# Performance work log

Hardware: AMD Instinct MI355X
Metric: run time of the kernel (lower is better)

## Reference

```python
import jax, jax.numpy as jnp
import numpy as np

B = 4096      # number of queries
N = 65536     # number of reference points

def setup_inputs() -> dict:
    key = jax.random.key(0)
    k1, k2, k3 = jax.random.split(key, 3)
    x = jax.random.normal(k1, (B,), dtype=jnp.float32)
    input_tensor = jax.random.normal(k2, (N,), dtype=jnp.float32)
    accuracy_tensor = jax.random.uniform(k3, (N,), dtype=jnp.float32)
    return {"x": x, "input_tensor": input_tensor, "accuracy_tensor": accuracy_tensor}

def reference(x, input_tensor, accuracy_tensor):
    # (B, N) broadcast abs-difference distance matrix
    distances = jnp.abs(input_tensor[None, :] - x[:, None])
    # nearest reference point per query
    min_idx = jnp.argmin(distances, axis=1)          # (B,)
    return accuracy_tensor[min_idx]                  # (B,)
```

## Files before the change

### kernel.cpp

```cpp
#include <hip/hip_runtime.h>

#define CHUNK 512
#define GRP   32
#define Q     2
#define QB    4

__global__ __launch_bounds__(256, 8)
void nn_init_kernel(unsigned long long* __restrict__ best, int B) {
    int i = blockIdx.x * 256 + threadIdx.x;
    if (i < B) best[i] = ~0ULL;
}

__global__ __launch_bounds__(256, 8)
void nn_main_kernel(const float* __restrict__ x,
                    const float* __restrict__ pts,
                    unsigned long long* __restrict__ best,
                    int qg_shift)
{
    __shared__ float lds[CHUNK];
    const int tid = threadIdx.x;
    const int qg = blockIdx.x & ((1 << qg_shift) - 1);
    const int ck = blockIdx.x >> qg_shift;

    reinterpret_cast<float2*>(lds)[tid] =
        reinterpret_cast<const float2*>(pts)[ck * (CHUNK / 2) + tid];

    const int q0 = (qg << 9) + tid;
    const float xq0 = x[q0];
    const float xq1 = x[q0 + 256];

    __syncthreads();

    const float inf = __builtin_inff();
    float bdA0 = inf, bdB0 = inf, prev0 = inf;
    float bdA1 = inf, bdB1 = inf, prev1 = inf;
    int grp0 = 0, grp1 = 0;

    const float4* __restrict__ l4 = reinterpret_cast<const float4*>(lds);

    #pragma unroll 2
    for (int g = 0; g < CHUNK / GRP; ++g) {
        #pragma unroll
        for (int t = 0; t < GRP / 4; ++t) {
            float4 v = l4[g * (GRP / 4) + t];
            bdA0 = fminf(fminf(fabsf(v.x - xq0), fabsf(v.y - xq0)), bdA0);
            bdB0 = fminf(fminf(fabsf(v.z - xq0), fabsf(v.w - xq0)), bdB0);
            bdA1 = fminf(fminf(fabsf(v.x - xq1), fabsf(v.y - xq1)), bdA1);
            bdB1 = fminf(fminf(fabsf(v.z - xq1), fabsf(v.w - xq1)), bdB1);
        }
        float cur0 = fminf(bdA0, bdB0);
        float cur1 = fminf(bdA1, bdB1);
        grp0 = (cur0 < prev0) ? g : grp0;  prev0 = cur0;
        grp1 = (cur1 < prev1) ? g : grp1;  prev1 = cur1;
    }

    int bi0 = 0, bi1 = 0;
    const float4* __restrict__ pg0 = l4 + grp0 * (GRP / 4);
    const float4* __restrict__ pg1 = l4 + grp1 * (GRP / 4);
    #pragma unroll
    for (int t = GRP / 4 - 1; t >= 0; --t) {
        float4 v = pg0[t];
        bi0 = (fabsf(v.w - xq0) == prev0) ? 4 * t + 3 : bi0;
        bi0 = (fabsf(v.z - xq0) == prev0) ? 4 * t + 2 : bi0;
        bi0 = (fabsf(v.y - xq0) == prev0) ? 4 * t + 1 : bi0;
        bi0 = (fabsf(v.x - xq0) == prev0) ? 4 * t + 0 : bi0;
    }
    #pragma unroll
    for (int t = GRP / 4 - 1; t >= 0; --t) {
        float4 v = pg1[t];
        bi1 = (fabsf(v.w - xq1) == prev1) ? 4 * t + 3 : bi1;
        bi1 = (fabsf(v.z - xq1) == prev1) ? 4 * t + 2 : bi1;
        bi1 = (fabsf(v.y - xq1) == prev1) ? 4 * t + 1 : bi1;
        bi1 = (fabsf(v.x - xq1) == prev1) ? 4 * t + 0 : bi1;
    }

    const unsigned base = (unsigned)(ck * CHUNK);
    const unsigned long long key0 =
        ((unsigned long long)__float_as_uint(prev0) << 32) |
        (base + (unsigned)(grp0 * GRP + bi0));
    const unsigned long long key1 =
        ((unsigned long long)__float_as_uint(prev1) << 32) |
        (base + (unsigned)(grp1 * GRP + bi1));
    atomicMin(&best[q0], key0);
    atomicMin(&best[q0 + 256], key1);
}

__global__ __launch_bounds__(256, 8)
void nn_gather_kernel(const unsigned long long* __restrict__ best,
                      const float* __restrict__ acc,
                      float* __restrict__ out, int B) {
    int i = blockIdx.x * 256 + threadIdx.x;
    if (i < B) out[i] = acc[(unsigned)(best[i] & 0xffffffffULL)];
}

__global__ __launch_bounds__(256, 4)
void nn_kernel(const float* __restrict__ x,
               const float* __restrict__ pts,
               const float* __restrict__ acc,
               float* __restrict__ out,
               int B, int N) {
    const int lane = threadIdx.x & 63;
    const int wave = threadIdx.x >> 6;
    const int q    = blockIdx.x * QB + wave;
    if (q >= B) return;

    const float xq = x[q];
    const int G = N >> 2;
    const int J = G >> 6;

    float bd0 = __builtin_inff(), bd1 = __builtin_inff(),
          bd2 = __builtin_inff(), bd3 = __builtin_inff();
    int   bj0 = 0, bj1 = 0, bj2 = 0, bj3 = 0;

    const float4* __restrict__ p4 = reinterpret_cast<const float4*>(pts);

    #pragma unroll 4
    for (int j = 0; j < J; ++j) {
        float4 v = p4[lane + 64 * j];
        float d0 = fabsf(v.x - xq);
        float d1 = fabsf(v.y - xq);
        float d2 = fabsf(v.z - xq);
        float d3 = fabsf(v.w - xq);
        if (d0 < bd0) { bd0 = d0; bj0 = j; }
        if (d1 < bd1) { bd1 = d1; bj1 = j; }
        if (d2 < bd2) { bd2 = d2; bj2 = j; }
        if (d3 < bd3) { bd3 = d3; bj3 = j; }
    }

    unsigned long long key;
    {
        unsigned i0 = (unsigned)(4 * (lane + 64 * bj0) + 0);
        unsigned i1 = (unsigned)(4 * (lane + 64 * bj1) + 1);
        unsigned i2 = (unsigned)(4 * (lane + 64 * bj2) + 2);
        unsigned i3 = (unsigned)(4 * (lane + 64 * bj3) + 3);
        unsigned long long k0 = ((unsigned long long)__float_as_uint(bd0) << 32) | i0;
        unsigned long long k1 = ((unsigned long long)__float_as_uint(bd1) << 32) | i1;
        unsigned long long k2 = ((unsigned long long)__float_as_uint(bd2) << 32) | i2;
        unsigned long long k3 = ((unsigned long long)__float_as_uint(bd3) << 32) | i3;
        key = k0 < k1 ? k0 : k1;
        unsigned long long k23 = k2 < k3 ? k2 : k3;
        key = key < k23 ? key : k23;
    }

    for (int i = J * 256 + lane; i < N; i += 64) {
        float d = fabsf(pts[i] - xq);
        unsigned long long k = ((unsigned long long)__float_as_uint(d) << 32) | (unsigned)i;
        key = key < k ? key : k;
    }

    #pragma unroll
    for (int off = 1; off < 64; off <<= 1) {
        unsigned long long o = __shfl_xor(key, off, 64);
        key = key < o ? key : o;
    }

    if (lane == 0) {
        out[q] = acc[(unsigned)(key & 0xffffffffULL)];
    }
}

extern "C" void kernel_launch(void* const* d_in, const int* in_sizes, int n_in,
                              void* d_out, int out_size, void* d_ws, size_t ws_size,
                              hipStream_t stream) {
    const float* x   = (const float*)d_in[0];
    const float* pts = (const float*)d_in[1];
    const float* acc = (const float*)d_in[2];
    float* out = (float*)d_out;
    const int B = in_sizes[0];
    const int N = in_sizes[1];

    const int nqg = B >> 9;
    const bool pow2 = (nqg > 0) && ((nqg & (nqg - 1)) == 0);
    const bool fast = pow2 && (B % 512 == 0) && (N % CHUNK == 0) &&
                      d_ws != nullptr && ws_size >= (size_t)B * 8;

    if (fast) {
        int qg_shift = 0;
        while ((1 << qg_shift) < nqg) ++qg_shift;
        const int nchunk = N / CHUNK;
        unsigned long long* best = (unsigned long long*)d_ws;

        hipLaunchKernelGGL(nn_init_kernel, dim3((B + 255) / 256), dim3(256), 0,
                           stream, best, B);
        hipLaunchKernelGGL(nn_main_kernel, dim3(nchunk * nqg), dim3(256), 0,
                           stream, x, pts, best, qg_shift);
        hipLaunchKernelGGL(nn_gather_kernel, dim3((B + 255) / 256), dim3(256),
                           0, stream, best, acc, out, B);
    } else {
        const int blocks = (B + QB - 1) / QB;
        hipLaunchKernelGGL(nn_kernel, dim3(blocks), dim3(256), 0, stream,
                           x, pts, acc, out, B, N);
    }
}
```

Before: 71.88 us.

## Replace global atomicMin with per-chunk partial buffer and separate reduction kernel

The main kernel now writes each chunk's best key into a per-chunk partial array instead of doing 64-bit atomicMin on a shared best array, and a new reduce kernel scans all chunks per query and gathers the accuracy value. This drops the init kernel and the atomic contention but requires nchunk*B*8 bytes of workspace, 128 chunks times 4096 queries, about 4 MB. The reduce kernel launches only 64 blocks of 64 threads, each thread doing 128 serial loads, so it may be latency bound. If the workspace is too small the fast path is not taken and the slow fallback kernel runs.

```diff
diff --git a/kernel.cpp b/kernel.cpp
--- a/kernel.cpp
+++ b/kernel.cpp
@@ -2,20 +2,13 @@
 
 #define CHUNK 512
 #define GRP   32
-#define Q     2
 #define QB    4
 
-__global__ __launch_bounds__(256, 8)
-void nn_init_kernel(unsigned long long* __restrict__ best, int B) {
-    int i = blockIdx.x * 256 + threadIdx.x;
-    if (i < B) best[i] = ~0ULL;
-}
-
-__global__ __launch_bounds__(256, 8)
+__global__ __launch_bounds__(256, 4)
 void nn_main_kernel(const float* __restrict__ x,
                     const float* __restrict__ pts,
-                    unsigned long long* __restrict__ best,
-                    int qg_shift)
+                    unsigned long long* __restrict__ part,
+                    int B, int qg_shift)
 {
     __shared__ float lds[CHUNK];
     const int tid = threadIdx.x;
@@ -81,16 +74,27 @@
     const unsigned long long key1 =
         ((unsigned long long)__float_as_uint(prev1) << 32) |
         (base + (unsigned)(grp1 * GRP + bi1));
-    atomicMin(&best[q0], key0);
-    atomicMin(&best[q0 + 256], key1);
+
+    part[(size_t)ck * B + q0]       = key0;
+    part[(size_t)ck * B + q0 + 256] = key1;
 }
 
-__global__ __launch_bounds__(256, 8)
-void nn_gather_kernel(const unsigned long long* __restrict__ best,
+__global__ __launch_bounds__(64, 8)
+void nn_reduce_kernel(const unsigned long long* __restrict__ part,
                       const float* __restrict__ acc,
-                      float* __restrict__ out, int B) {
-    int i = blockIdx.x * 256 + threadIdx.x;
-    if (i < B) out[i] = acc[(unsigned)(best[i] & 0xffffffffULL)];
+                      float* __restrict__ out,
+                      int B, int nchunk)
+{
+    const int q = blockIdx.x * 64 + threadIdx.x;
+    if (q >= B) return;
+
+    unsigned long long key = ~0ULL;
+    #pragma unroll 8
+    for (int c = 0; c < nchunk; ++c) {
+        unsigned long long k = part[(size_t)c * B + q];
+        key = k < key ? k : key;
+    }
+    out[q] = acc[(unsigned)(key & 0xffffffffULL)];
 }
 
 __global__ __launch_bounds__(256, 4)
@@ -170,22 +174,21 @@
     const int N = in_sizes[1];
 
     const int nqg = B >> 9;
+    const int nchunk = N / CHUNK;
     const bool pow2 = (nqg > 0) && ((nqg & (nqg - 1)) == 0);
     const bool fast = pow2 && (B % 512 == 0) && (N % CHUNK == 0) &&
-                      d_ws != nullptr && ws_size >= (size_t)B * 8;
+                      d_ws != nullptr &&
+                      ws_size >= (size_t)nchunk * (size_t)B * 8;
 
     if (fast) {
         int qg_shift = 0;
         while ((1 << qg_shift) < nqg) ++qg_shift;
-        const int nchunk = N / CHUNK;
-        unsigned long long* best = (unsigned long long*)d_ws;
+        unsigned long long* part = (unsigned long long*)d_ws;
 
-        hipLaunchKernelGGL(nn_init_kernel, dim3((B + 255) / 256), dim3(256), 0,
-                           stream, best, B);
         hipLaunchKernelGGL(nn_main_kernel, dim3(nchunk * nqg), dim3(256), 0,
-                           stream, x, pts, best, qg_shift);
-        hipLaunchKernelGGL(nn_gather_kernel, dim3((B + 255) / 256), dim3(256),
-                           0, stream, best, acc, out, B);
+                           stream, x, pts, part, B, qg_shift);
+        hipLaunchKernelGGL(nn_reduce_kernel, dim3((B + 63) / 64), dim3(64), 0,
+                           stream, part, acc, out, B, nchunk);
     } else {
         const int blocks = (B + QB - 1) / QB;
         hipLaunchKernelGGL(nn_kernel, dim3(blocks), dim3(256), 0, stream,
```

Measured after the change: 75.43 us. 1.05x slower.
